# Performance work log

Measured on AMD Instinct MI355X. Metric: run time of the kernel, lower is better.

The kernel has to match this reference:

```python
import jax, jax.numpy as jnp
import numpy as np

E = 1024   # embed_dim
H = 16     # num_heads
NQ = 8     # ffn_dim == n_qubits
B, S = 2, 2048


def setup_inputs() -> dict:
    key = jax.random.key(0)
    ks = jax.random.split(key, 8)
    g = lambda k, sh, sc=1.0: jax.random.normal(k, sh, jnp.float32) * sc
    return {
        "x": g(ks[0], (B, S, E)),
        "w_qkv": g(ks[1], (3 * E, E), 0.02),      # nn.Linear(E, 3E, bias=False).weight
        "w_comb": g(ks[2], (E, E), 0.02),          # combine Linear weight
        "b_comb": jnp.zeros((E,), jnp.float32),
        "gamma1": jnp.ones((E,), jnp.float32),     # norm1
        "beta1": jnp.zeros((E,), jnp.float32),
        "gamma2": jnp.ones((E,), jnp.float32),     # norm2
        "beta2": jnp.zeros((E,), jnp.float32),
        "theta": g(ks[3], (NQ,)),                  # trainable RY angles
        "w1": g(ks[4], (1, NQ), 0.3),              # linear1 weight [1, n_qubits]
        "b1": jnp.zeros((1,), jnp.float32),
    }


def _layernorm(x, g, b, eps=1e-5):
    m = jnp.mean(x, axis=-1, keepdims=True)
    v = jnp.var(x, axis=-1, keepdims=True)
    return (x - m) * jax.lax.rsqrt(v + eps) * g + b


def reference(x, w_qkv, w_comb, b_comb, gamma1, beta1, gamma2, beta2, theta, w1, b1):
    Bx, Sx, Em = x.shape
    dk = Em // H
    # ---- attention ----
    qkv = (x @ w_qkv.T).reshape(Bx, Sx, 3, H, dk)
    q = jnp.transpose(qkv[:, :, 0], (0, 2, 1, 3))  # [B,H,S,dk]
    k = jnp.transpose(qkv[:, :, 1], (0, 2, 1, 3))
    v = jnp.transpose(qkv[:, :, 2], (0, 2, 1, 3))
    scores = jnp.einsum('bhqd,bhkd->bhqk', q, k) / jnp.sqrt(jnp.float32(dk))
    probs = jax.nn.softmax(scores, axis=-1)        # dropout = identity (eval)
    out = jnp.einsum('bhqk,bhkd->bhqd', probs, v)
    out = jnp.transpose(out, (0, 2, 1, 3)).reshape(Bx, Sx, Em)
    attn = out @ w_comb.T + b_comb
    x1 = _layernorm(x + attn, gamma1, beta1)
    # ---- quantum FFN: RX(x_i) encode, RY(theta_i), <Z_i> = cos(theta_i)*cos(x_i) ----
    z = jnp.cos(x1[..., :theta.shape[0]]) * jnp.cos(theta)  # [B,S,NQ]
    ffn = z @ w1.T + b1                                      # [B,S,1], broadcasts
    return _layernorm(x1 + ffn, gamma2, beta2)
```

## Files before the change

kernel.cpp:

```cpp
#include <hip/hip_runtime.h>
#include <hip/hip_bf16.h>
#include <math.h>

typedef __bf16 bf16;
typedef bf16 bf16x8 __attribute__((ext_vector_type(8)));
typedef bf16 bf16x4 __attribute__((ext_vector_type(4)));
typedef float f32x4 __attribute__((ext_vector_type(4)));
typedef unsigned int u32;

#define EMB 1024
#define NH 16
#define DK 64
#define SEQ 2048
#define NB 2
#define NTOK (NB*SEQ)

#define QSCALE 0.18033688011112043f

#if defined(__has_builtin)
#if __has_builtin(__builtin_amdgcn_exp2f)
#define EXP2(x) __builtin_amdgcn_exp2f(x)
#else
#define EXP2(x) exp2f(x)
#endif
#else
#define EXP2(x) exp2f(x)
#endif

__device__ __forceinline__ void gl_lds16(const void* g, void* l) {
    __builtin_amdgcn_global_load_lds(
        (const __attribute__((address_space(1))) u32*)g,
        (__attribute__((address_space(3))) u32*)l, 16, 0, 0);
}

#define SWZ(row, colblk) (((row)*64) + ((((colblk) ^ ((row)&7)))*8))

#define PSTR 72

__device__ __forceinline__ void xcd_remap(int gx, int* bx, int* by) {
    int gy  = gridDim.y;
    int nwg = gx * gy;
    int wg  = *by * gx + *bx;
    int per = nwg >> 3;
    int s   = (wg & 7) * per + (wg >> 3);
    *bx = s % gx;
    *by = s / gx;
}

__global__ __launch_bounds__(256) void convert3(
    const float* __restrict__ s0, const float* __restrict__ s1,
    const float* __restrict__ s2,
    bf16* __restrict__ d0, bf16* __restrict__ d1, bf16* __restrict__ d2)
{
    const float* src; bf16* dst; int n;
    switch (blockIdx.y) {
        case 0:  src = s0; dst = d0; n = NTOK*EMB;  break;
        case 1:  src = s1; dst = d1; n = 3*EMB*EMB; break;
        default: src = s2; dst = d2; n = EMB*EMB;   break;
    }
    int i = (blockIdx.x * 256 + threadIdx.x) * 8;
    if (i + 7 < n) {
        float4 a = *(const float4*)(src + i);
        float4 b = *(const float4*)(src + i + 4);
        bf16x8 o;
        o[0] = (bf16)a.x; o[1] = (bf16)a.y; o[2] = (bf16)a.z; o[3] = (bf16)a.w;
        o[4] = (bf16)b.x; o[5] = (bf16)b.y; o[6] = (bf16)b.z; o[7] = (bf16)b.w;
        *(bf16x8*)(dst + i) = o;
    }
}

template<int MODE, int BM>
__global__ __launch_bounds__(256) void gemm_bt(
    const bf16* __restrict__ Aa, const bf16* __restrict__ Bb,
    bf16* __restrict__ qb, bf16* __restrict__ kb, bf16* __restrict__ vtb,
    float* __restrict__ outc, int Kdim)
{
    constexpr int MI = BM / 32;
    __shared__ __align__(16) bf16 At0[BM*64];
    __shared__ __align__(16) bf16 At1[BM*64];
    __shared__ __align__(16) bf16 Bt0[128*64];
    __shared__ __align__(16) bf16 Bt1[128*64];
    const int tid  = threadIdx.x;
    const int w    = tid >> 6, lane = tid & 63;
    const int quad = lane >> 4, l15 = lane & 15;
    const int wr   = w >> 1,   wc  = w & 1;
    int bx = blockIdx.x, by = blockIdx.y;
    xcd_remap(gridDim.x, &bx, &by);
    const int m0 = by * BM, n0 = bx * 128;
    const int lrow = lane >> 3;
    const int lswz = ((lane & 7) ^ lrow) * 8;

    f32x4 acc[MI][4] = {};

    auto stageAB = [&](int k0, bf16* At, bf16* Bt) {
        #pragma unroll
        for (int i = 0; i < MI; ++i) {
            int r = w*(BM/4) + i*8 + lrow;
            gl_lds16(Aa + (size_t)(m0 + r)*Kdim + k0 + lswz, At + (w*(BM/4) + i*8)*64);
        }
        #pragma unroll
        for (int i = 0; i < 4; ++i) {
            int r = w*32 + i*8 + lrow;
            gl_lds16(Bb + (size_t)(n0 + r)*Kdim + k0 + lswz, Bt + (w*32 + i*8)*64);
        }
    };

    auto computeAB = [&](const bf16* At, const bf16* Bt) {
        #pragma unroll
        for (int kk = 0; kk < 2; ++kk) {
            bf16x8 a[MI], b[4];
            #pragma unroll
            for (int i = 0; i < MI; ++i)
                a[i] = *(const bf16x8*)(At + SWZ(wr*(BM/2) + i*16 + l15, 4*kk + quad));
            #pragma unroll
            for (int j = 0; j < 4; ++j)
                b[j] = *(const bf16x8*)(Bt + SWZ(wc*64 + j*16 + l15, 4*kk + quad));
            __builtin_amdgcn_s_setprio(1);
            #pragma unroll
            for (int i = 0; i < MI; ++i)
                #pragma unroll
                for (int j = 0; j < 4; ++j)
                    acc[i][j] = __builtin_amdgcn_mfma_f32_16x16x32_bf16(a[i], b[j], acc[i][j], 0, 0, 0);
            __builtin_amdgcn_s_setprio(0);
        }
    };

    const int NT2 = Kdim >> 7;
    stageAB(0, At0, Bt0);
    for (int t2 = 0; t2 < NT2; ++t2) {
        __syncthreads();
        stageAB(t2*128 + 64, At1, Bt1);
        computeAB(At0, Bt0);
        __syncthreads();
        if (t2 + 1 < NT2)
            stageAB(t2*128 + 128, At0, Bt0);
        computeAB(At1, Bt1);
    }

    for (int i = 0; i < MI; ++i) for (int j = 0; j < 4; ++j) {
        int rb  = m0 + wr*(BM/2) + i*16 + quad*4;
        int col = n0 + wc*64 + j*16 + l15;
        if (MODE == 0) {
            int c = col >> 10, h = (col >> 6) & 15, d = col & 63;
            int b_ = rb >> 11, s = rb & 2047;
            int bh = b_*NH + h;
            if (c == 2) {
                bf16 tmp[4] __attribute__((aligned(8)));
                for (int r = 0; r < 4; ++r) tmp[r] = (bf16)acc[i][j][r];
                *(ushort4*)(vtb + ((size_t)bh*DK + d)*SEQ + s) = *(ushort4*)tmp;
            } else if (c == 0) {
                for (int r = 0; r < 4; ++r)
                    qb[((size_t)bh*SEQ + s + r)*DK + d] = (bf16)(acc[i][j][r] * QSCALE);
            } else {
                for (int r = 0; r < 4; ++r)
                    kb[((size_t)bh*SEQ + s + r)*DK + d] = (bf16)acc[i][j][r];
            }
        } else {
            for (int r = 0; r < 4; ++r)
                outc[(size_t)(rb + r)*EMB + col] = acc[i][j][r];
        }
    }
}

__global__ __launch_bounds__(256) void attn_kernel(
    const bf16* __restrict__ q, const bf16* __restrict__ k,
    const bf16* __restrict__ vt, bf16* __restrict__ out)
{
    __shared__ __align__(16) bf16 QP[4*32*PSTR];
    __shared__ __align__(16) bf16 Kt0[64*64];
    __shared__ __align__(16) bf16 Kt1[64*64];
    __shared__ __align__(16) bf16 Vt0[64*64];
    __shared__ __align__(16) bf16 Vt1[64*64];

    const int tid  = threadIdx.x;
    const int w    = tid >> 6, lane = tid & 63;
    const int quad = lane >> 4, l15 = lane & 15;
    int qt = blockIdx.x, bh = blockIdx.y;
    xcd_remap(gridDim.x, &qt, &bh);
    const int lrow = lane >> 3;
    const int lswz = ((lane & 7) ^ lrow) * 8;

    for (int i = 0; i < 4; ++i) {
        int r = w*32 + i*8 + lrow;
        gl_lds16(q + ((size_t)bh*SEQ + qt*128 + r)*DK + lswz, QP + (w*32 + i*8)*64);
    }
    asm volatile("s_waitcnt vmcnt(0)" ::: "memory");

    bf16x8 qf[2][2];
    for (int rt = 0; rt < 2; ++rt)
        for (int kk = 0; kk < 2; ++kk)
            qf[rt][kk] = *(const bf16x8*)(QP + SWZ(w*32 + rt*16 + l15, 4*kk + quad));

    bf16* Pw = QP + w * 32 * PSTR;

    f32x4 O[2][4] = {};
    float psum[2] = {};

    auto stage_kv = [&](int kt, bf16* Kb, bf16* Vb) {
        #pragma unroll
        for (int i = 0; i < 2; ++i) {
            int r = w*16 + i*8 + lrow;
            gl_lds16(k  + ((size_t)bh*SEQ + kt*64 + r)*DK + lswz, Kb + (w*16 + i*8)*64);
            gl_lds16(vt + ((size_t)bh*DK + r)*SEQ + kt*64 + lswz, Vb + (w*16 + i*8)*64);
        }
    };

    auto compute = [&](const bf16* Kb, const bf16* Vb) {
        f32x4 sc[2][4] = {};
        for (int kk = 0; kk < 2; ++kk) {
            bf16x8 kf[4];
            #pragma unroll
            for (int j = 0; j < 4; ++j)
                kf[j] = *(const bf16x8*)(Kb + SWZ(j*16 + l15, 4*kk + quad));
            __builtin_amdgcn_s_setprio(1);
            #pragma unroll
            for (int j = 0; j < 4; ++j) {
                sc[0][j] = __builtin_amdgcn_mfma_f32_16x16x32_bf16(kf[j], qf[0][kk], sc[0][j], 0, 0, 0);
                sc[1][j] = __builtin_amdgcn_mfma_f32_16x16x32_bf16(kf[j], qf[1][kk], sc[1][j], 0, 0, 0);
            }
            __builtin_amdgcn_s_setprio(0);
        }
        #pragma unroll
        for (int rt = 0; rt < 2; ++rt)
            #pragma unroll
            for (int j = 0; j < 4; ++j) {
                bf16x4 pk;
                #pragma unroll
                for (int r = 0; r < 4; ++r) {
                    float p = EXP2(sc[rt][j][r]);
                    psum[rt] += p;
                    pk[r] = (bf16)p;
                }
                *(bf16x4*)(Pw + (rt*16 + l15)*PSTR + j*16 + quad*4) = pk;
            }
        asm volatile("s_waitcnt lgkmcnt(0)" ::: "memory");
        for (int kk = 0; kk < 2; ++kk) {
            bf16x8 vb[4];
            #pragma unroll
            for (int j = 0; j < 4; ++j)
                vb[j] = *(const bf16x8*)(Vb + SWZ(j*16 + l15, 4*kk + quad));
            bf16x8 a0 = *(const bf16x8*)(Pw + (     l15)*PSTR + kk*32 + quad*8);
            bf16x8 a1 = *(const bf16x8*)(Pw + (16 + l15)*PSTR + kk*32 + quad*8);
            __builtin_amdgcn_s_setprio(1);
            #pragma unroll
            for (int j = 0; j < 4; ++j) {
                O[0][j] = __builtin_amdgcn_mfma_f32_16x16x32_bf16(a0, vb[j], O[0][j], 0, 0, 0);
                O[1][j] = __builtin_amdgcn_mfma_f32_16x16x32_bf16(a1, vb[j], O[1][j], 0, 0, 0);
            }
            __builtin_amdgcn_s_setprio(0);
        }
    };

    stage_kv(0, Kt0, Vt0);
    for (int kt2 = 0; kt2 < SEQ/128; ++kt2) {
        __syncthreads();
        stage_kv(2*kt2 + 1, Kt1, Vt1);
        compute(Kt0, Vt0);
        __syncthreads();
        if (kt2 + 1 < SEQ/128)
            stage_kv(2*kt2 + 2, Kt0, Vt0);
        compute(Kt1, Vt1);
    }

    float inv[2][4];
    #pragma unroll
    for (int rt = 0; rt < 2; ++rt) {
        float s = psum[rt];
        s += __shfl_xor(s, 16, 64);
        s += __shfl_xor(s, 32, 64);
        #pragma unroll
        for (int r = 0; r < 4; ++r)
            inv[rt][r] = 1.f / __shfl(s, quad*4 + r, 64);
    }

    const int b_ = bh >> 4, h = bh & 15;
    #pragma unroll
    for (int rt = 0; rt < 2; ++rt)
        #pragma unroll
        for (int j = 0; j < 4; ++j)
            #pragma unroll
            for (int r = 0; r < 4; ++r) {
                int t   = b_*SEQ + qt*128 + w*32 + rt*16 + quad*4 + r;
                int col = h*DK + j*16 + l15;
                out[(size_t)t*EMB + col] = (bf16)(O[rt][j][r] * inv[rt][r]);
            }
}

__global__ __launch_bounds__(256) void ln_kernel(
    const float* __restrict__ x, const float* __restrict__ comb,
    const float* __restrict__ bcomb,
    const float* __restrict__ g1, const float* __restrict__ be1,
    const float* __restrict__ g2, const float* __restrict__ be2,
    const float* __restrict__ theta, const float* __restrict__ w1v,
    const float* __restrict__ b1v, float* __restrict__ out)
{
    const int w    = threadIdx.x >> 6, lane = threadIdx.x & 63;
    const int t    = blockIdx.x * 4 + w;

    float r[4][4];
    float s = 0.f, ss = 0.f;
    #pragma unroll
    for (int c = 0; c < 4; ++c) {
        int e = c*256 + lane*4;
        float4 xv = *(const float4*)(x    + (size_t)t*EMB + e);
        float4 cv = *(const float4*)(comb + (size_t)t*EMB + e);
        float4 bv = *(const float4*)(bcomb + e);
        r[c][0] = xv.x + cv.x + bv.x; r[c][1] = xv.y + cv.y + bv.y;
        r[c][2] = xv.z + cv.z + bv.z; r[c][3] = xv.w + cv.w + bv.w;
        #pragma unroll
        for (int i = 0; i < 4; ++i) { s += r[c][i]; ss += r[c][i]*r[c][i]; }
    }
    #pragma unroll
    for (int m = 1; m < 64; m <<= 1) { s += __shfl_xor(s, m, 64); ss += __shfl_xor(ss, m, 64); }
    float mean = s * (1.f/1024.f);
    float var  = ss * (1.f/1024.f) - mean*mean;
    float inv  = rsqrtf(var + 1e-5f);

    float x1[4][4];
    #pragma unroll
    for (int c = 0; c < 4; ++c) {
        int e = c*256 + lane*4;
        #pragma unroll
        for (int i = 0; i < 4; ++i)
            x1[c][i] = (r[c][i] - mean)*inv*g1[e+i] + be1[e+i];
    }

    float pf = 0.f;
    if (lane < 2) {
        #pragma unroll
        for (int i = 0; i < 4; ++i) {
            int e = lane*4 + i;
            pf += cosf(x1[0][i]) * cosf(theta[e]) * w1v[e];
        }
    }
    pf += __shfl_xor(pf, 1, 64);
    float f = __shfl(pf, 0, 64) + b1v[0];

    float s2 = 0.f, ss2 = 0.f;
    #pragma unroll
    for (int c = 0; c < 4; ++c)
        #pragma unroll
        for (int i = 0; i < 4; ++i) {
            float v2 = x1[c][i] + f; s2 += v2; ss2 += v2*v2;
        }
    #pragma unroll
    for (int m = 1; m < 64; m <<= 1) { s2 += __shfl_xor(s2, m, 64); ss2 += __shfl_xor(ss2, m, 64); }
    float mean2 = s2 * (1.f/1024.f);
    float var2  = ss2 * (1.f/1024.f) - mean2*mean2;
    float inv2  = rsqrtf(var2 + 1e-5f);

    #pragma unroll
    for (int c = 0; c < 4; ++c) {
        int e = c*256 + lane*4;
        float4 ov;
        ov.x = ((x1[c][0] + f) - mean2)*inv2*g2[e+0] + be2[e+0];
        ov.y = ((x1[c][1] + f) - mean2)*inv2*g2[e+1] + be2[e+1];
        ov.z = ((x1[c][2] + f) - mean2)*inv2*g2[e+2] + be2[e+2];
        ov.w = ((x1[c][3] + f) - mean2)*inv2*g2[e+3] + be2[e+3];
        *(float4*)(out + (size_t)t*EMB + e) = ov;
    }
}

extern "C" void kernel_launch(void* const* d_in, const int* in_sizes, int n_in,
                              void* d_out, int out_size, void* d_ws, size_t ws_size,
                              hipStream_t stream)
{
    const float* x      = (const float*)d_in[0];
    const float* w_qkv  = (const float*)d_in[1];
    const float* w_comb = (const float*)d_in[2];
    const float* b_comb = (const float*)d_in[3];
    const float* g1     = (const float*)d_in[4];
    const float* be1    = (const float*)d_in[5];
    const float* g2     = (const float*)d_in[6];
    const float* be2    = (const float*)d_in[7];
    const float* theta  = (const float*)d_in[8];
    const float* w1v    = (const float*)d_in[9];
    const float* b1v    = (const float*)d_in[10];
    float* out = (float*)d_out;

    char* ws = (char*)d_ws;
    bf16*  xb     = (bf16*)(ws);
    bf16*  wqkvb  = (bf16*)(ws + ( 8u<<20));
    bf16*  wcombb = (bf16*)(ws + (14u<<20));
    bf16*  qb     = (bf16*)(ws + (16u<<20));
    bf16*  kb     = (bf16*)(ws + (24u<<20));
    bf16*  vtb    = (bf16*)(ws + (32u<<20));
    bf16*  attn   = (bf16*)(ws + (40u<<20));
    float* comb   = (float*)(ws + (16u<<20));

    convert3<<<dim3(2048, 3), 256, 0, stream>>>(x, w_qkv, w_comb, xb, wqkvb, wcombb);

    gemm_bt<0,128><<<dim3(3*EMB/128, NTOK/128), 256, 0, stream>>>(
        xb, wqkvb, qb, kb, vtb, nullptr, EMB);
    attn_kernel<<<dim3(SEQ/128, NB*NH), 256, 0, stream>>>(qb, kb, vtb, attn);
    gemm_bt<1,64><<<dim3(EMB/128, NTOK/64), 256, 0, stream>>>(
        attn, wcombb, nullptr, nullptr, nullptr, comb, EMB);
    ln_kernel<<<NTOK/4, 256, 0, stream>>>(x, comb, b_comb, g1, be1, g2, be2,
                                          theta, w1v, b1v, out);
}
```

Baseline: 206.1 us.

## Switch attention to 32x32x16 MFMA and keep P in registers via permlane swap

Result: faster. 195.3 us (-5.2%).

```diff
diff --git a/kernel.cpp b/kernel.cpp
--- a/kernel.cpp
+++ b/kernel.cpp
@@ -6,7 +6,9 @@
 typedef bf16 bf16x8 __attribute__((ext_vector_type(8)));
 typedef bf16 bf16x4 __attribute__((ext_vector_type(4)));
 typedef float f32x4 __attribute__((ext_vector_type(4)));
+typedef float f32x16 __attribute__((ext_vector_type(16)));
 typedef unsigned int u32;
+typedef unsigned int u32x2v __attribute__((ext_vector_type(2)));
 
 #define EMB 1024
 #define NH 16
@@ -35,8 +37,6 @@
 
 #define SWZ(row, colblk) (((row)*64) + ((((colblk) ^ ((row)&7)))*8))
 
-#define PSTR 72
-
 __device__ __forceinline__ void xcd_remap(int gx, int* bx, int* by) {
     int gy  = gridDim.y;
     int nwg = gx * gy;
@@ -45,6 +45,25 @@
     int s   = (wg & 7) * per + (wg >> 3);
     *bx = s % gx;
     *by = s / gx;
+}
+
+__device__ __forceinline__ u32 cvtpk(float a, float b) {
+    u32 r;
+    asm("v_cvt_pk_bf16_f32 %0, %1, %2" : "=v"(r) : "v"(a), "v"(b));
+    return r;
+}
+
+__device__ __forceinline__ void plswap(u32 x, u32 y, u32* ox, u32* oy) {
+#if defined(__has_builtin) && __has_builtin(__builtin_amdgcn_permlane32_swap)
+    u32x2v r = __builtin_amdgcn_permlane32_swap(x, y, false, false);
+    *ox = r.x; *oy = r.y;
+#else
+    u32 xs = (u32)__shfl_xor((int)x, 32, 64);
+    u32 ys = (u32)__shfl_xor((int)y, 32, 64);
+    bool hi = (threadIdx.x & 32) != 0;
+    *ox = hi ? ys : x;
+    *oy = hi ? y : xs;
+#endif
 }
 
 __global__ __launch_bounds__(256) void convert3(
@@ -166,7 +185,7 @@
     const bf16* __restrict__ q, const bf16* __restrict__ k,
     const bf16* __restrict__ vt, bf16* __restrict__ out)
 {
-    __shared__ __align__(16) bf16 QP[4*32*PSTR];
+    __shared__ __align__(16) bf16 QP[128*64];
     __shared__ __align__(16) bf16 Kt0[64*64];
     __shared__ __align__(16) bf16 Kt1[64*64];
     __shared__ __align__(16) bf16 Vt0[64*64];
@@ -174,7 +193,7 @@
 
     const int tid  = threadIdx.x;
     const int w    = tid >> 6, lane = tid & 63;
-    const int quad = lane >> 4, l15 = lane & 15;
+    const int l31  = lane & 31, hi = lane >> 5;
     int qt = blockIdx.x, bh = blockIdx.y;
     xcd_remap(gridDim.x, &qt, &bh);
     const int lrow = lane >> 3;
@@ -186,15 +205,13 @@
     }
     asm volatile("s_waitcnt vmcnt(0)" ::: "memory");
 
-    bf16x8 qf[2][2];
-    for (int rt = 0; rt < 2; ++rt)
-        for (int kk = 0; kk < 2; ++kk)
-            qf[rt][kk] = *(const bf16x8*)(QP + SWZ(w*32 + rt*16 + l15, 4*kk + quad));
-
-    bf16* Pw = QP + w * 32 * PSTR;
-
-    f32x4 O[2][4] = {};
-    float psum[2] = {};
+    bf16x8 qf[4];
+    #pragma unroll
+    for (int m = 0; m < 4; ++m)
+        qf[m] = *(const bf16x8*)(QP + SWZ(w*32 + l31, m*2 + hi));
+
+    f32x16 O[2] = {};
+    float psum = 0.f;
 
     auto stage_kv = [&](int kt, bf16* Kb, bf16* Vb) {
         #pragma unroll
@@ -206,48 +223,42 @@
     };
 
     auto compute = [&](const bf16* Kb, const bf16* Vb) {
-        f32x4 sc[2][4] = {};
-        for (int kk = 0; kk < 2; ++kk) {
-            bf16x8 kf[4];
-            #pragma unroll
-            for (int j = 0; j < 4; ++j)
-                kf[j] = *(const bf16x8*)(Kb + SWZ(j*16 + l15, 4*kk + quad));
+        f32x16 sc[2] = {};
+        #pragma unroll
+        for (int m = 0; m < 4; ++m) {
+            bf16x8 kf0 = *(const bf16x8*)(Kb + SWZ(     l31, m*2 + hi));
+            bf16x8 kf1 = *(const bf16x8*)(Kb + SWZ(32 + l31, m*2 + hi));
             __builtin_amdgcn_s_setprio(1);
-            #pragma unroll
-            for (int j = 0; j < 4; ++j) {
-                sc[0][j] = __builtin_amdgcn_mfma_f32_16x16x32_bf16(kf[j], qf[0][kk], sc[0][j], 0, 0, 0);
-                sc[1][j] = __builtin_amdgcn_mfma_f32_16x16x32_bf16(kf[j], qf[1][kk], sc[1][j], 0, 0, 0);
+            sc[0] = __builtin_amdgcn_mfma_f32_32x32x16_bf16(kf0, qf[m], sc[0], 0, 0, 0);
+            sc[1] = __builtin_amdgcn_mfma_f32_32x32x16_bf16(kf1, qf[m], sc[1], 0, 0, 0);
+            __builtin_amdgcn_s_setprio(0);
+        }
+        #pragma unroll
+        for (int kvt = 0; kvt < 2; ++kvt) {
+            float p[16];
+            #pragma unroll
+            for (int r = 0; r < 16; ++r) {
+                p[r] = EXP2(sc[kvt][r]);
+                psum += p[r];
             }
-            __builtin_amdgcn_s_setprio(0);
-        }
-        #pragma unroll
-        for (int rt = 0; rt < 2; ++rt)
-            #pragma unroll
-            for (int j = 0; j < 4; ++j) {
-                bf16x4 pk;
-                #pragma unroll
-                for (int r = 0; r < 4; ++r) {
-                    float p = EXP2(sc[rt][j][r]);
-                    psum[rt] += p;
-                    pk[r] = (bf16)p;
-                }
-                *(bf16x4*)(Pw + (rt*16 + l15)*PSTR + j*16 + quad*4) = pk;
+            u32 pw[8];
+            #pragma unroll
+            for (int i = 0; i < 8; ++i)
+                pw[i] = cvtpk(p[2*i], p[2*i+1]);
+            union { u32 u[4]; bf16x8 v; } A1, A2;
+            plswap(pw[0], pw[2], &A1.u[0], &A1.u[2]);
+            plswap(pw[1], pw[3], &A1.u[1], &A1.u[3]);
+            plswap(pw[4], pw[6], &A2.u[0], &A2.u[2]);
+            plswap(pw[5], pw[7], &A2.u[1], &A2.u[3]);
+            #pragma unroll
+            for (int dt = 0; dt < 2; ++dt) {
+                bf16x8 vb1 = *(const bf16x8*)(Vb + SWZ(dt*32 + l31, kvt*4 + 0 + hi));
+                bf16x8 vb2 = *(const bf16x8*)(Vb + SWZ(dt*32 + l31, kvt*4 + 2 + hi));
+                __builtin_amdgcn_s_setprio(1);
+                O[dt] = __builtin_amdgcn_mfma_f32_32x32x16_bf16(A1.v, vb1, O[dt], 0, 0, 0);
+                O[dt] = __builtin_amdgcn_mfma_f32_32x32x16_bf16(A2.v, vb2, O[dt], 0, 0, 0);
+                __builtin_amdgcn_s_setprio(0);
             }
-        asm volatile("s_waitcnt lgkmcnt(0)" ::: "memory");
-        for (int kk = 0; kk < 2; ++kk) {
-            bf16x8 vb[4];
-            #pragma unroll
-            for (int j = 0; j < 4; ++j)
-                vb[j] = *(const bf16x8*)(Vb + SWZ(j*16 + l15, 4*kk + quad));
-            bf16x8 a0 = *(const bf16x8*)(Pw + (     l15)*PSTR + kk*32 + quad*8);
-            bf16x8 a1 = *(const bf16x8*)(Pw + (16 + l15)*PSTR + kk*32 + quad*8);
-            __builtin_amdgcn_s_setprio(1);
-            #pragma unroll
-            for (int j = 0; j < 4; ++j) {
-                O[0][j] = __builtin_amdgcn_mfma_f32_16x16x32_bf16(a0, vb[j], O[0][j], 0, 0, 0);
-                O[1][j] = __builtin_amdgcn_mfma_f32_16x16x32_bf16(a1, vb[j], O[1][j], 0, 0, 0);
-            }
-            __builtin_amdgcn_s_setprio(0);
         }
     };
 
@@ -262,28 +273,24 @@
         compute(Kt1, Vt1);
     }
 
-    float inv[2][4];
-    #pragma unroll
-    for (int rt = 0; rt < 2; ++rt) {
-        float s = psum[rt];
-        s += __shfl_xor(s, 16, 64);
-        s += __shfl_xor(s, 32, 64);
-        #pragma unroll
-        for (int r = 0; r < 4; ++r)
-            inv[rt][r] = 1.f / __shfl(s, quad*4 + r, 64);
+    float s = psum + __shfl_xor(psum, 32, 64);
+    float inv[16];
+    #pragma unroll
+    for (int r = 0; r < 16; ++r) {
+        int qrow = (r & 3) + 8*(r >> 2) + 4*hi;
+        inv[r] = 1.f / __shfl(s, qrow, 64);
     }
 
     const int b_ = bh >> 4, h = bh & 15;
     #pragma unroll
-    for (int rt = 0; rt < 2; ++rt)
-        #pragma unroll
-        for (int j = 0; j < 4; ++j)
-            #pragma unroll
-            for (int r = 0; r < 4; ++r) {
-                int t   = b_*SEQ + qt*128 + w*32 + rt*16 + quad*4 + r;
-                int col = h*DK + j*16 + l15;
-                out[(size_t)t*EMB + col] = (bf16)(O[rt][j][r] * inv[rt][r]);
-            }
+    for (int dt = 0; dt < 2; ++dt)
+        #pragma unroll
+        for (int r = 0; r < 16; ++r) {
+            int qrow = (r & 3) + 8*(r >> 2) + 4*hi;
+            int t    = b_*SEQ + qt*128 + w*32 + qrow;
+            int col  = h*DK + dt*32 + l31;
+            out[(size_t)t*EMB + col] = (bf16)(O[dt][r] * inv[r]);
+        }
 }
 
 __global__ __launch_bounds__(256) void ln_kernel(
```
